# Optimization experiments

Hardware: AMD Instinct MI355X
Metric: run time of the kernel (lower is better)

Reference implementation:

```python
import jax, jax.numpy as jnp
import numpy as np

B, N = 16384, 2048
L = 1.0  # regularizer scale `l`


def setup_inputs() -> dict:
    key = jax.random.key(0)
    w = jax.random.normal(key, (B, N), dtype=jnp.float32)
    return {"w": w}


def reference(w):
    # Standardize each unit (column) over the batch; K.std is population std.
    mean = jnp.mean(w, axis=0)
    std = jnp.std(w, axis=0)
    fs = (w - mean) / std  # [B, N]

    # Original: for all P = N*(N-1)/2 pairs (i<j), loss_xy[b] = |mean_pairs(fs[b,i]*fs[b,j])|
    # (note K.mean axis=0 on the gathered [P, B] arrays reduces over PAIRS, per batch element).
    # Use the exact identity sum_{i<j} x_i x_j = ((sum x)^2 - sum x^2) / 2
    # to avoid materializing the O(N^2) gathered pairs.
    n = w.shape[1]
    s = jnp.sum(fs, axis=1)        # [B]
    s2 = jnp.sum(fs * fs, axis=1)  # [B]
    pair_mean = (s * s - s2) / (n * (n - 1))  # == sum_pairs / P, shape [B]

    return L * jnp.mean(jnp.abs(pair_mean))
```

## Files before the change

### kernel.cpp

```cpp
#include <hip/hip_runtime.h>
#include <math.h>

#define B_ROWS 16384
#define N_COLS 2048

#define WS_PART     0
#define WS_GRP      (1024 * 4096)
#define WS_MEAN     (WS_GRP + 16 * 4096)
#define WS_INVSTD   (WS_MEAN + N_COLS)
#define WS_RP       (WS_INVSTD + N_COLS)

constexpr int K1_ROWCHUNKS = 1024;
constexpr int K1_ROWS = B_ROWS / K1_ROWCHUNKS;

__global__ __launch_bounds__(256) void colstats_kernel(
    const float* __restrict__ w, float* __restrict__ part) {
  const int cg = blockIdx.x & 1;
  const int rc = blockIdx.x >> 1;
  const int col4 = cg * 256 + threadIdx.x;
  const float4* __restrict__ w4 = reinterpret_cast<const float4*>(w) + col4;
  const size_t stride = N_COLS / 4;
  const size_t base = (size_t)rc * K1_ROWS * stride;

  float sx = 0.f, sy = 0.f, sz = 0.f, sw = 0.f;
  float qx = 0.f, qy = 0.f, qz = 0.f, qw = 0.f;
#pragma unroll
  for (int batch = 0; batch < K1_ROWS / 8; ++batch) {
    float4 v[8];
#pragma unroll
    for (int i = 0; i < 8; ++i)
      v[i] = w4[base + (size_t)(batch * 8 + i) * stride];
#pragma unroll
    for (int i = 0; i < 8; ++i) {
      sx += v[i].x; sy += v[i].y; sz += v[i].z; sw += v[i].w;
      qx = fmaf(v[i].x, v[i].x, qx);
      qy = fmaf(v[i].y, v[i].y, qy);
      qz = fmaf(v[i].z, v[i].z, qz);
      qw = fmaf(v[i].w, v[i].w, qw);
    }
  }
  float4* __restrict__ p4 = reinterpret_cast<float4*>(part);
  p4[(size_t)rc * 1024 + col4] = make_float4(sx, sy, sz, sw);
  p4[(size_t)rc * 1024 + 512 + col4] = make_float4(qx, qy, qz, qw);
}

__global__ __launch_bounds__(256) void reduce1_kernel(
    const float* __restrict__ part, float* __restrict__ grp) {
  const int t = blockIdx.x * 256 + threadIdx.x;
  const int g = t >> 10;
  const int pos = t & 1023;
  const float4* __restrict__ p4 = reinterpret_cast<const float4*>(part);
  float ax = 0.f, ay = 0.f, az = 0.f, aw = 0.f;
  for (int b = 0; b < 8; ++b) {
    float4 v[8];
#pragma unroll
    for (int i = 0; i < 8; ++i)
      v[i] = p4[(size_t)(g * 64 + b * 8 + i) * 1024 + pos];
#pragma unroll
    for (int i = 0; i < 8; ++i) {
      ax += v[i].x; ay += v[i].y; az += v[i].z; aw += v[i].w;
    }
  }
  reinterpret_cast<float4*>(grp)[(size_t)g * 1024 + pos] =
      make_float4(ax, ay, az, aw);
}

__global__ __launch_bounds__(256) void finalize_kernel(
    const float* __restrict__ grp, float* __restrict__ ws) {
  const int n = blockIdx.x * 256 + threadIdx.x;
  float s = 0.f, q = 0.f;
#pragma unroll
  for (int g = 0; g < 16; ++g) {
    s += grp[g * 4096 + n];
    q += grp[g * 4096 + 2048 + n];
  }
  const float inv_b = 1.0f / (float)B_ROWS;
  float mean = s * inv_b;
  float var = q * inv_b - mean * mean;
  ws[WS_MEAN + n] = mean;
  ws[WS_INVSTD + n] = 1.0f / sqrtf(var);
}

constexpr int K3_BLOCKS = 2048;
constexpr int ROWS_PER_BLOCK = B_ROWS / K3_BLOCKS;

__global__ __launch_bounds__(256) void rowpass_kernel(
    const float* __restrict__ w, const float* __restrict__ ws,
    float* __restrict__ partials) {
  __shared__ float4 sm_mean[N_COLS / 4];
  __shared__ float4 sm_inv[N_COLS / 4];
  __shared__ float warpsum[4];

  const float4* __restrict__ g_mean = reinterpret_cast<const float4*>(ws + WS_MEAN);
  const float4* __restrict__ g_inv = reinterpret_cast<const float4*>(ws + WS_INVSTD);
  for (int i = threadIdx.x; i < N_COLS / 4; i += 256) {
    sm_mean[i] = g_mean[i];
    sm_inv[i] = g_inv[i];
  }
  __syncthreads();

  const int wid = threadIdx.x >> 6;
  const int lane = threadIdx.x & 63;
  constexpr float inv_pairs = 1.0f / ((float)N_COLS * (float)(N_COLS - 1));

  const int row_a = blockIdx.x * ROWS_PER_BLOCK + wid * 2;
  const float4* __restrict__ ra =
      reinterpret_cast<const float4*>(w + (size_t)row_a * N_COLS);
  const float4* __restrict__ rb =
      reinterpret_cast<const float4*>(w + (size_t)(row_a + 1) * N_COLS);

  float4 va[8], vb[8];
#pragma unroll
  for (int k = 0; k < 8; ++k) va[k] = ra[lane + k * 64];
#pragma unroll
  for (int k = 0; k < 8; ++k) vb[k] = rb[lane + k * 64];

  float sa = 0.f, qa = 0.f, sb = 0.f, qb = 0.f;
#pragma unroll
  for (int k = 0; k < 8; ++k) {
    const int idx = lane + k * 64;
    float4 m = sm_mean[idx];
    float4 iv = sm_inv[idx];
    float ax = (va[k].x - m.x) * iv.x, ay = (va[k].y - m.y) * iv.y;
    float az = (va[k].z - m.z) * iv.z, aw = (va[k].w - m.w) * iv.w;
    float bx = (vb[k].x - m.x) * iv.x, by = (vb[k].y - m.y) * iv.y;
    float bz = (vb[k].z - m.z) * iv.z, bw = (vb[k].w - m.w) * iv.w;
    sa += (ax + ay) + (az + aw);
    qa += fmaf(ax, ax, fmaf(ay, ay, fmaf(az, az, aw * aw)));
    sb += (bx + by) + (bz + bw);
    qb += fmaf(bx, bx, fmaf(by, by, fmaf(bz, bz, bw * bw)));
  }
#pragma unroll
  for (int off = 32; off > 0; off >>= 1) {
    sa += __shfl_xor(sa, off);
    qa += __shfl_xor(qa, off);
    sb += __shfl_xor(sb, off);
    qb += __shfl_xor(qb, off);
  }
  float pm_a = (sa * sa - qa) * inv_pairs;
  float pm_b = (sb * sb - qb) * inv_pairs;
  float acc = fabsf(pm_a) + fabsf(pm_b);

  if (lane == 0) warpsum[wid] = acc;
  __syncthreads();
  if (threadIdx.x == 0)
    partials[blockIdx.x] = (warpsum[0] + warpsum[1]) + (warpsum[2] + warpsum[3]);
}

__global__ __launch_bounds__(256) void final_reduce_kernel(
    const float* __restrict__ partials, float* __restrict__ out) {
  __shared__ float warpsum[4];
  float acc = 0.f;
  for (int i = threadIdx.x; i < K3_BLOCKS; i += 256) acc += partials[i];
#pragma unroll
  for (int off = 32; off > 0; off >>= 1) acc += __shfl_xor(acc, off);
  const int wid = threadIdx.x >> 6;
  const int lane = threadIdx.x & 63;
  if (lane == 0) warpsum[wid] = acc;
  __syncthreads();
  if (threadIdx.x == 0) {
    float total = (warpsum[0] + warpsum[1]) + (warpsum[2] + warpsum[3]);
    out[0] = total * (1.0f / (float)B_ROWS);
  }
}

extern "C" void kernel_launch(void* const* d_in, const int* in_sizes, int n_in,
                              void* d_out, int out_size, void* d_ws, size_t ws_size,
                              hipStream_t stream) {
  const float* w = reinterpret_cast<const float*>(d_in[0]);
  float* out = reinterpret_cast<float*>(d_out);
  float* ws = reinterpret_cast<float*>(d_ws);

  colstats_kernel<<<K1_ROWCHUNKS * 2, 256, 0, stream>>>(w, ws + WS_PART);
  reduce1_kernel<<<64, 256, 0, stream>>>(ws + WS_PART, ws + WS_GRP);
  finalize_kernel<<<8, 256, 0, stream>>>(ws + WS_GRP, ws);
  rowpass_kernel<<<K3_BLOCKS, 256, 0, stream>>>(w, ws, ws + WS_RP);
  final_reduce_kernel<<<1, 256, 0, stream>>>(ws + WS_RP, out);
}
```

Measured before the change: 222.0 us.

## Fuse column-stat reductions into one kernel and rebalance row pass occupancy

Merges the two-stage partial reduction and finalize kernels into a single stats_reduce kernel that reduces all 1024 row-chunk partials per column with shuffles and shared memory, then writes mean and inverse std directly. This removes one launch and the intermediate group buffer round trip. It also adds occupancy hints (launch_bounds with 8 blocks) and limits unrolling in colstats to cut register pressure. The row pass now handles one row per wave with twice as many blocks, which trades per-thread memory parallelism for more resident waves.

After: 223.7 us. Within noise of the previous version (+0.7%).

```diff
diff --git a/kernel.cpp b/kernel.cpp
--- a/kernel.cpp
+++ b/kernel.cpp
@@ -5,15 +5,14 @@
 #define N_COLS 2048
 
 #define WS_PART     0
-#define WS_GRP      (1024 * 4096)
-#define WS_MEAN     (WS_GRP + 16 * 4096)
+#define WS_MEAN     (1024 * 4096)
 #define WS_INVSTD   (WS_MEAN + N_COLS)
 #define WS_RP       (WS_INVSTD + N_COLS)
 
 constexpr int K1_ROWCHUNKS = 1024;
 constexpr int K1_ROWS = B_ROWS / K1_ROWCHUNKS;
 
-__global__ __launch_bounds__(256) void colstats_kernel(
+__global__ __launch_bounds__(256, 8) void colstats_kernel(
     const float* __restrict__ w, float* __restrict__ part) {
   const int cg = blockIdx.x & 1;
   const int rc = blockIdx.x >> 1;
@@ -24,7 +23,7 @@
 
   float sx = 0.f, sy = 0.f, sz = 0.f, sw = 0.f;
   float qx = 0.f, qy = 0.f, qz = 0.f, qw = 0.f;
-#pragma unroll
+#pragma unroll 1
   for (int batch = 0; batch < K1_ROWS / 8; ++batch) {
     float4 v[8];
 #pragma unroll
@@ -44,47 +43,66 @@
   p4[(size_t)rc * 1024 + 512 + col4] = make_float4(qx, qy, qz, qw);
 }
 
-__global__ __launch_bounds__(256) void reduce1_kernel(
-    const float* __restrict__ part, float* __restrict__ grp) {
-  const int t = blockIdx.x * 256 + threadIdx.x;
-  const int g = t >> 10;
-  const int pos = t & 1023;
+__global__ __launch_bounds__(256) void stats_reduce_kernel(
+    const float* __restrict__ part, float* __restrict__ ws) {
+  const int tid = threadIdx.x;
+  const int c4 = blockIdx.x * 4 + (tid & 3);
+  const int sub = tid >> 2;
   const float4* __restrict__ p4 = reinterpret_cast<const float4*>(part);
-  float ax = 0.f, ay = 0.f, az = 0.f, aw = 0.f;
-  for (int b = 0; b < 8; ++b) {
-    float4 v[8];
+
+  float4 s = make_float4(0.f, 0.f, 0.f, 0.f);
+  float4 q = make_float4(0.f, 0.f, 0.f, 0.f);
+#pragma unroll 1
+  for (int i = 0; i < 16; ++i) {
+    const int rc = sub * 16 + i;
+    float4 a = p4[(size_t)rc * 1024 + c4];
+    float4 b = p4[(size_t)rc * 1024 + 512 + c4];
+    s.x += a.x; s.y += a.y; s.z += a.z; s.w += a.w;
+    q.x += b.x; q.y += b.y; q.z += b.z; q.w += b.w;
+  }
 #pragma unroll
-    for (int i = 0; i < 8; ++i)
-      v[i] = p4[(size_t)(g * 64 + b * 8 + i) * 1024 + pos];
+  for (int off = 4; off <= 32; off <<= 1) {
+    s.x += __shfl_xor(s.x, off); s.y += __shfl_xor(s.y, off);
+    s.z += __shfl_xor(s.z, off); s.w += __shfl_xor(s.w, off);
+    q.x += __shfl_xor(q.x, off); q.y += __shfl_xor(q.y, off);
+    q.z += __shfl_xor(q.z, off); q.w += __shfl_xor(q.w, off);
+  }
+  __shared__ float4 red_s[4][4];
+  __shared__ float4 red_q[4][4];
+  const int wid = tid >> 6;
+  const int lane = tid & 63;
+  if (lane < 4) {
+    red_s[wid][lane] = s;
+    red_q[wid][lane] = q;
+  }
+  __syncthreads();
+  if (tid < 4) {
+    float4 S = red_s[0][tid], Q = red_q[0][tid];
 #pragma unroll
-    for (int i = 0; i < 8; ++i) {
-      ax += v[i].x; ay += v[i].y; az += v[i].z; aw += v[i].w;
+    for (int w_ = 1; w_ < 4; ++w_) {
+      S.x += red_s[w_][tid].x; S.y += red_s[w_][tid].y;
+      S.z += red_s[w_][tid].z; S.w += red_s[w_][tid].w;
+      Q.x += red_q[w_][tid].x; Q.y += red_q[w_][tid].y;
+      Q.z += red_q[w_][tid].z; Q.w += red_q[w_][tid].w;
     }
+    const float inv_b = 1.0f / (float)B_ROWS;
+    float4 mean, inv;
+    mean.x = S.x * inv_b; mean.y = S.y * inv_b;
+    mean.z = S.z * inv_b; mean.w = S.w * inv_b;
+    inv.x = 1.0f / sqrtf(Q.x * inv_b - mean.x * mean.x);
+    inv.y = 1.0f / sqrtf(Q.y * inv_b - mean.y * mean.y);
+    inv.z = 1.0f / sqrtf(Q.z * inv_b - mean.z * mean.z);
+    inv.w = 1.0f / sqrtf(Q.w * inv_b - mean.w * mean.w);
+    const int c4o = blockIdx.x * 4 + tid;
+    reinterpret_cast<float4*>(ws + WS_MEAN)[c4o] = mean;
+    reinterpret_cast<float4*>(ws + WS_INVSTD)[c4o] = inv;
   }
-  reinterpret_cast<float4*>(grp)[(size_t)g * 1024 + pos] =
-      make_float4(ax, ay, az, aw);
 }
 
-__global__ __launch_bounds__(256) void finalize_kernel(
-    const float* __restrict__ grp, float* __restrict__ ws) {
-  const int n = blockIdx.x * 256 + threadIdx.x;
-  float s = 0.f, q = 0.f;
-#pragma unroll
-  for (int g = 0; g < 16; ++g) {
-    s += grp[g * 4096 + n];
-    q += grp[g * 4096 + 2048 + n];
-  }
-  const float inv_b = 1.0f / (float)B_ROWS;
-  float mean = s * inv_b;
-  float var = q * inv_b - mean * mean;
-  ws[WS_MEAN + n] = mean;
-  ws[WS_INVSTD + n] = 1.0f / sqrtf(var);
-}
-
-constexpr int K3_BLOCKS = 2048;
+constexpr int K3_BLOCKS = 4096;
 constexpr int ROWS_PER_BLOCK = B_ROWS / K3_BLOCKS;
 
-__global__ __launch_bounds__(256) void rowpass_kernel(
+__global__ __launch_bounds__(256, 8) void rowpass_kernel(
     const float* __restrict__ w, const float* __restrict__ ws,
     float* __restrict__ partials) {
   __shared__ float4 sm_mean[N_COLS / 4];
@@ -93,9 +111,11 @@
 
   const float4* __restrict__ g_mean = reinterpret_cast<const float4*>(ws + WS_MEAN);
   const float4* __restrict__ g_inv = reinterpret_cast<const float4*>(ws + WS_INVSTD);
-  for (int i = threadIdx.x; i < N_COLS / 4; i += 256) {
-    sm_mean[i] = g_mean[i];
-    sm_inv[i] = g_inv[i];
+#pragma unroll
+  for (int i = 0; i < 2; ++i) {
+    const int idx = threadIdx.x + i * 256;
+    sm_mean[idx] = g_mean[idx];
+    sm_inv[idx] = g_inv[idx];
   }
   __syncthreads();
 
@@ -103,19 +123,15 @@
   const int lane = threadIdx.x & 63;
   constexpr float inv_pairs = 1.0f / ((float)N_COLS * (float)(N_COLS - 1));
 
-  const int row_a = blockIdx.x * ROWS_PER_BLOCK + wid * 2;
-  const float4* __restrict__ ra =
-      reinterpret_cast<const float4*>(w + (size_t)row_a * N_COLS);
-  const float4* __restrict__ rb =
-      reinterpret_cast<const float4*>(w + (size_t)(row_a + 1) * N_COLS);
+  const int row = blockIdx.x * ROWS_PER_BLOCK + wid;
+  const float4* __restrict__ rp =
+      reinterpret_cast<const float4*>(w + (size_t)row * N_COLS);
 
-  float4 va[8], vb[8];
+  float4 va[8];
 #pragma unroll
-  for (int k = 0; k < 8; ++k) va[k] = ra[lane + k * 64];
-#pragma unroll
-  for (int k = 0; k < 8; ++k) vb[k] = rb[lane + k * 64];
+  for (int k = 0; k < 8; ++k) va[k] = rp[lane + k * 64];
 
-  float sa = 0.f, qa = 0.f, sb = 0.f, qb = 0.f;
+  float s = 0.f, q = 0.f;
 #pragma unroll
   for (int k = 0; k < 8; ++k) {
     const int idx = lane + k * 64;
@@ -123,25 +139,18 @@
     float4 iv = sm_inv[idx];
     float ax = (va[k].x - m.x) * iv.x, ay = (va[k].y - m.y) * iv.y;
     float az = (va[k].z - m.z) * iv.z, aw = (va[k].w - m.w) * iv.w;
-    float bx = (vb[k].x - m.x) * iv.x, by = (vb[k].y - m.y) * iv.y;
-    float bz = (vb[k].z - m.z) * iv.z, bw = (vb[k].w - m.w) * iv.w;
-    sa += (ax + ay) + (az + aw);
-    qa += fmaf(ax, ax, fmaf(ay, ay, fmaf(az, az, aw * aw)));
-    sb += (bx + by) + (bz + bw);
-    qb += fmaf(bx, bx, fmaf(by, by, fmaf(bz, bz, bw * bw)));
+    s += (ax + ay) + (az + aw);
+    q += fmaf(ax, ax, fmaf(ay, ay, fmaf(az, az, aw * aw)));
   }
 #pragma unroll
   for (int off = 32; off > 0; off >>= 1) {
-    sa += __shfl_xor(sa, off);
-    qa += __shfl_xor(qa, off);
-    sb += __shfl_xor(sb, off);
-    qb += __shfl_xor(qb, off);
+    s += __shfl_xor(s, off);
+    q += __shfl_xor(q, off);
   }
-  float pm_a = (sa * sa - qa) * inv_pairs;
-  float pm_b = (sb * sb - qb) * inv_pairs;
-  float acc = fabsf(pm_a) + fabsf(pm_b);
-
-  if (lane == 0) warpsum[wid] = acc;
+  if (lane == 0) {
+    float pm = (s * s - q) * inv_pairs;
+    warpsum[wid] = fabsf(pm);
+  }
   __syncthreads();
   if (threadIdx.x == 0)
     partials[blockIdx.x] = (warpsum[0] + warpsum[1]) + (warpsum[2] + warpsum[3]);
@@ -172,8 +181,7 @@
   float* ws = reinterpret_cast<float*>(d_ws);
 
   colstats_kernel<<<K1_ROWCHUNKS * 2, 256, 0, stream>>>(w, ws + WS_PART);
-  reduce1_kernel<<<64, 256, 0, stream>>>(ws + WS_PART, ws + WS_GRP);
-  finalize_kernel<<<8, 256, 0, stream>>>(ws + WS_GRP, ws);
+  stats_reduce_kernel<<<128, 256, 0, stream>>>(ws + WS_PART, ws);
   rowpass_kernel<<<K3_BLOCKS, 256, 0, stream>>>(w, ws, ws + WS_RP);
   final_reduce_kernel<<<1, 256, 0, stream>>>(ws + WS_RP, out);
 }
```
